# Performance work log

Measured on AMD Instinct MI355X. Metric: run time of the kernel, lower is better.

Reference implementation:

```python
import jax, jax.numpy as jnp
import numpy as np

B = 1024
N_CPGS = 20000
N_FREQS = N_CPGS // 2 + 1  # 10001
HIDDEN = (256, 128, 64)
LN_EPS = 1e-5


def setup_inputs() -> dict:
    key = jax.random.key(0)
    keys = jax.random.split(key, 16)
    inp = {"x": jax.random.normal(keys[0], (B, N_CPGS), dtype=jnp.float32)}
    in_dim = N_FREQS
    for i, h in enumerate(HIDDEN):
        inp[f"W{i}"] = jax.random.normal(keys[1 + i], (h, in_dim), dtype=jnp.float32) * 0.01
        inp[f"alpha{i}"] = jnp.full((h, in_dim), 0.01, dtype=jnp.float32)
        inp[f"b{i}"] = jnp.zeros((h,), dtype=jnp.float32)
        inp[f"eta{i}"] = jnp.asarray(0.1, dtype=jnp.float32)
        inp[f"g{i}"] = jnp.ones((h,), dtype=jnp.float32)   # LayerNorm gamma
        inp[f"be{i}"] = jnp.zeros((h,), dtype=jnp.float32)  # LayerNorm beta
        in_dim = h
    inp["head_w"] = jax.random.normal(keys[10], (1, in_dim), dtype=jnp.float32) * (1.0 / np.sqrt(in_dim))
    inp["head_b"] = jnp.zeros((1,), dtype=jnp.float32)
    return inp


def _hebbian_layer(x, W, alpha, b, eta):
    # y_slow = x W^T + b;  plastic[b,i] = eta * tanh(y_slow)[b,i] * sum_j sigmoid(alpha)[i,j] * x_norm[b,j] * x[b,j]
    y_slow = jnp.einsum('bd,hd->bh', x, W) + b
    x_norm = x / (jnp.linalg.norm(x, axis=-1, keepdims=True) + 1e-8)
    c = x_norm * x  # (B, in) -- collapses the (B,out,in) outer-product trace algebraically
    plastic = eta * jnp.tanh(y_slow) * jnp.einsum('bd,hd->bh', c, jax.nn.sigmoid(alpha))
    return y_slow + plastic


def _layer_norm(h, g, be):
    mu = jnp.mean(h, axis=-1, keepdims=True)
    var = jnp.mean((h - mu) ** 2, axis=-1, keepdims=True)
    return (h - mu) * jax.lax.rsqrt(var + LN_EPS) * g + be


def reference(x, W0, alpha0, b0, eta0, g0, be0,
              W1, alpha1, b1, eta1, g1, be1,
              W2, alpha2, b2, eta2, g2, be2,
              head_w, head_b):
    # FFT spectral front-end
    xc = x - jnp.mean(x, axis=1, keepdims=True)
    h = jnp.log1p(jnp.abs(jnp.fft.rfft(xc, axis=1)))  # (B, N_FREQS)
    params = [(W0, alpha0, b0, eta0, g0, be0),
              (W1, alpha1, b1, eta1, g1, be1),
              (W2, alpha2, b2, eta2, g2, be2)]
    for (W, a, b, eta, g, be) in params:
        h = jax.nn.gelu(_layer_norm(_hebbian_layer(h, W, a, b, eta), g, be), approximate=False)
        # dropout is identity in eval mode
    return (jnp.einsum('bd,od->bo', h, head_w) + head_b)[:, 0]  # (B,)
```

## Files before the change

kernel.cpp:

```cpp
#include <hip/hip_runtime.h>
#include <hip/hip_bf16.h>
#include <math.h>

typedef short bf16x8 __attribute__((ext_vector_type(8)));
typedef float f32x4 __attribute__((ext_vector_type(4)));

static __device__ __forceinline__ unsigned short f2bf(float f) {
    unsigned int u = __float_as_uint(f);
    unsigned int r = (u + 0x7fffu + ((u >> 16) & 1u)) >> 16;
    return (unsigned short)r;
}

static __device__ __forceinline__ bf16x8 sq_bf16x8(bf16x8 a) {
    bf16x8 r;
    #pragma unroll
    for (int i = 0; i < 8; ++i) {
        unsigned int u = ((unsigned int)(unsigned short)a[i]) << 16;
        float f = __uint_as_float(u);
        f *= f;
        r[i] = (short)f2bf(f);
    }
    return r;
}

static __device__ __forceinline__ float gelu_f(float x) {
    return 0.5f * x * (1.f + erff(x * 0.70710678118654752f));
}

static __device__ __forceinline__ void gload_lds16(const void* g, void* l) {
    __builtin_amdgcn_global_load_lds(
        (const __attribute__((address_space(1))) unsigned int*)g,
        (__attribute__((address_space(3))) unsigned int*)l, 16, 0, 0);
}

static __device__ __forceinline__ int ldsmap(int i) { return i + (i >> 6); }

static __device__ __forceinline__ int rev4(int k) {
    int d0 = k % 10; k /= 10;
    int d1 = k % 10; k /= 10;
    int d2 = k % 10; int d3 = k / 10;
    return d0 * 1000 + d1 * 100 + d2 * 10 + d3;
}

__global__ __launch_bounds__(256)
void init_tables_kernel(unsigned int* __restrict__ idxTab, float2* __restrict__ twAll)
{
    int i = blockIdx.x * 256 + threadIdx.x;
    if (i < 10001) {
        int k1 = (i == 10000) ? 0 : i;
        int k2 = (k1 == 0) ? 0 : 10000 - k1;
        unsigned a = (unsigned)ldsmap(rev4(k1));
        unsigned b = (unsigned)ldsmap(rev4(k2));
        idxTab[i] = a | (b << 16);
    }
    if (i < 9990) {
        int m;
        if (i < 9000)       { int t = i / 1000 + 1; int j = i - (t - 1) * 1000; m = j * t; }
        else if (i < 9900)  { int e = i - 9000; int t = e / 100 + 1; int j = e - (t - 1) * 100; m = 10 * j * t; }
        else                { int e = i - 9900; int t = e / 10 + 1;  int j = e - (t - 1) * 10;  m = 100 * j * t; }
        double ang = (double)m * -6.2831853071795864769e-4;
        twAll[i] = make_float2((float)cos(ang), (float)sin(ang));
    }
}

static __device__ __forceinline__ void dft5(
    float a0r, float a0i, float a1r, float a1i, float a2r, float a2i,
    float a3r, float a3i, float a4r, float a4i,
    float* Xr, float* Xi)
{
    const float c1 = 0.30901699437494742f, c2 = -0.80901699437494745f;
    const float s1 = 0.95105651629515357f, s2 = 0.58778525229247312f;
    float t1r = a1r + a4r, t1i = a1i + a4i;
    float d1r = a1r - a4r, d1i = a1i - a4i;
    float t2r = a2r + a3r, t2i = a2i + a3i;
    float d2r = a2r - a3r, d2i = a2i - a3i;
    Xr[0] = a0r + t1r + t2r; Xi[0] = a0i + t1i + t2i;
    float m1r = a0r + c1 * t1r + c2 * t2r, m1i = a0i + c1 * t1i + c2 * t2i;
    float m2r = a0r + c2 * t1r + c1 * t2r, m2i = a0i + c2 * t1i + c1 * t2i;
    float n1r = s1 * d1r + s2 * d2r, n1i = s1 * d1i + s2 * d2i;
    float n2r = s2 * d1r - s1 * d2r, n2i = s2 * d1i - s1 * d2i;
    Xr[1] = m1r + n1i; Xi[1] = m1i - n1r;
    Xr[4] = m1r - n1i; Xi[4] = m1i + n1r;
    Xr[2] = m2r + n2i; Xi[2] = m2i - n2r;
    Xr[3] = m2r - n2i; Xi[3] = m2i + n2r;
}

template<int S>
static __device__ __forceinline__ void radix10_core(
    float* __restrict__ reb, float* __restrict__ imb,
    const float* ar, const float* ai, int base, int j,
    const float2* __restrict__ tw)
{
    constexpr int L  = (S == 0) ? 1000 : (S == 1) ? 100 : (S == 2) ? 10 : 1;
    constexpr bool TW = (S != 3);

    const float WR[5] = {1.f, 0.80901699437494745f, 0.30901699437494742f,
                         -0.30901699437494742f, -0.80901699437494745f};
    const float WI[5] = {0.f, -0.58778525229247312f, -0.95105651629515357f,
                         -0.95105651629515357f, -0.58778525229247312f};

    float Er[5], Ei[5], Or[5], Oi[5];
    dft5(ar[0], ai[0], ar[2], ai[2], ar[4], ai[4], ar[6], ai[6], ar[8], ai[8], Er, Ei);
    dft5(ar[1], ai[1], ar[3], ai[3], ar[5], ai[5], ar[7], ai[7], ar[9], ai[9], Or, Oi);
    #pragma unroll
    for (int k = 1; k < 5; ++k) {
        float tr = Or[k] * WR[k] - Oi[k] * WI[k];
        Oi[k] = Or[k] * WI[k] + Oi[k] * WR[k];
        Or[k] = tr;
    }

    if (TW) {
        float twr[10], twi[10];
        #pragma unroll
        for (int t = 1; t < 10; ++t) {
            float2 w_ = tw[(t - 1) * L + j];
            twr[t] = w_.x; twi[t] = w_.y;
        }
        #pragma unroll
        for (int k = 0; k < 5; ++k) {
            float xr0 = Er[k] + Or[k], xi0 = Ei[k] + Oi[k];
            float xr1 = Er[k] - Or[k], xi1 = Ei[k] - Oi[k];
            int i0 = ldsmap(base + k * L);
            int i1 = ldsmap(base + (k + 5) * L);
            if (k == 0) {
                reb[i0] = xr0;
                imb[i0] = xi0;
            } else {
                reb[i0] = xr0 * twr[k] - xi0 * twi[k];
                imb[i0] = xr0 * twi[k] + xi0 * twr[k];
            }
            reb[i1] = xr1 * twr[k + 5] - xi1 * twi[k + 5];
            imb[i1] = xr1 * twi[k + 5] + xi1 * twr[k + 5];
        }
    } else {
        #pragma unroll
        for (int k = 0; k < 5; ++k) {
            int i0 = ldsmap(base + k * L);
            int i1 = ldsmap(base + (k + 5) * L);
            reb[i0] = Er[k] + Or[k]; imb[i0] = Ei[k] + Oi[k];
            reb[i1] = Er[k] - Or[k]; imb[i1] = Ei[k] - Oi[k];
        }
    }
}

template<int S>
static __device__ __forceinline__ void radix10_stage(
    float* __restrict__ reb, float* __restrict__ imb, int tid,
    const float2* __restrict__ tw)
{
    constexpr int L = (S == 1) ? 100 : (S == 2) ? 10 : 1;
    for (int w = tid; w < 1000; w += 512) {
        int g, j;
        if (S == 3) { g = w; j = 0; }
        else        { g = w / L; j = w - g * L; }
        const int base = g * (10 * L) + j;
        float ar[10], ai[10];
        #pragma unroll
        for (int u = 0; u < 10; ++u) {
            int idx = ldsmap(base + u * L);
            ar[u] = reb[idx];
            ai[u] = imb[idx];
        }
        radix10_core<S>(reb, imb, ar, ai, base, j, tw);
    }
}

__global__ __launch_bounds__(512, 4)
void fft_prep_kernel(const float* __restrict__ x,
                     unsigned short* __restrict__ hb,
                     float* __restrict__ hnorm,
                     const float* __restrict__ W0, const float* __restrict__ A0,
                     unsigned short* __restrict__ Wb, unsigned short* __restrict__ Sb,
                     const float* __restrict__ W1, const float* __restrict__ A1,
                     const float* __restrict__ W2, const float* __restrict__ A2,
                     float* __restrict__ W1T, float* __restrict__ S1T,
                     float* __restrict__ W2T, float* __restrict__ S2T,
                     const unsigned int* __restrict__ idxTab,
                     const float2* __restrict__ twAll)
{
    if (blockIdx.x >= 1024) {
        int idx = (blockIdx.x - 1024) * 512 + threadIdx.x;
        if (idx < 1280128) {
            const bool isW = idx < 640064;
            const int f4 = isW ? idx : idx - 640064;
            const float* src = isW ? W0 : A0;
            unsigned short* dst = isW ? Wb : Sb;
            float4 v = ((const float4*)src)[f4];
            float e[4] = {v.x, v.y, v.z, v.w};
            int flat = f4 * 4;
            int row = flat / 10001;
            int col = flat - row * 10001;
            #pragma unroll
            for (int i = 0; i < 4; ++i) {
                if (col == 10001) { row++; col = 0; }
                float val = isW ? e[i] : 1.f / (1.f + expf(-e[i]));
                dst[(size_t)row * 10240 + col] = f2bf(val);
                col++;
            }
        } else if (idx < 1341312) {
            int i = idx - 1280128;
            int row = i / 239;
            int col = 10001 + (i - row * 239);
            Wb[(size_t)row * 10240 + col] = 0;
            Sb[(size_t)row * 10240 + col] = 0;
        } else if (idx < 1423232) {
            int o = idx - 1341312;
            if (o < 32768) {
                int d = o >> 7, h = o & 127;
                W1T[o] = W1[h * 256 + d];
            } else if (o < 65536) {
                int p = o - 32768;
                int d = p >> 7, h = p & 127;
                S1T[p] = 1.f / (1.f + expf(-A1[h * 256 + d]));
            } else if (o < 73728) {
                int p = o - 65536;
                int d = p >> 6, h = p & 63;
                W2T[p] = W2[h * 128 + d];
            } else {
                int p = o - 73728;
                int d = p >> 6, h = p & 63;
                S2T[p] = 1.f / (1.f + expf(-A2[h * 128 + d]));
            }
        }
        return;
    }

    __shared__ float reb[10156];
    __shared__ float imb[10156];
    __shared__ float redbuf[8];

    const int b = blockIdx.x;
    const int tid = threadIdx.x;
    const int lane = tid & 63;
    const int wv = tid >> 6;

    const float2* T0 = twAll;
    const float2* T1 = twAll + 9000;
    const float2* T2 = twAll + 9900;

    const float2* z2 = (const float2*)(x + (size_t)b * 20000);
    for (int w = tid; w < 1000; w += 512) {
        float ar[10], ai[10];
        #pragma unroll
        for (int u = 0; u < 10; ++u) {
            float2 v = z2[w + u * 1000];
            ar[u] = v.x; ai[u] = v.y;
        }
        radix10_core<0>(reb, imb, ar, ai, w, w, T0);
    }
    __syncthreads();
    radix10_stage<1>(reb, imb, tid, T1);
    __syncthreads();
    radix10_stage<2>(reb, imb, tid, T2);
    __syncthreads();
    radix10_stage<3>(reb, imb, tid, (const float2*)nullptr);
    __syncthreads();

    float ct, st;
    __sincosf((float)tid * -3.14159265358979324e-4f, &st, &ct);
    const float RC = 0.987091579f;
    const float RS = -0.160156842f;
    float sumsq = 0.f;
    unsigned short* hrow = hb + (size_t)b * 10240;
    #pragma unroll
    for (int i = 0; i < 20; ++i) {
        int k = tid + i * 512;
        float hval = 0.f;
        if (k > 0 && k <= 10000) {
            unsigned pp = idxTab[k];
            int i1 = (int)(pp & 0xffffu);
            int i2 = (int)(pp >> 16);
            float zr = reb[i1], zi = imb[i1];
            float wr = reb[i2], wi = imb[i2];
            float er = 0.5f * (zr + wr);
            float ei = 0.5f * (zi - wi);
            float odr = 0.5f * (zi + wi);
            float odi = -0.5f * (zr - wr);
            float xre = er + ct * odr - st * odi;
            float xim = ei + ct * odi + st * odr;
            hval = __logf(1.f + sqrtf(xre * xre + xim * xim));
        }
        hrow[k] = f2bf(hval);
        sumsq += hval * hval;
        float nct = ct * RC - st * RS;
        st = ct * RS + st * RC;
        ct = nct;
    }
    #pragma unroll
    for (int o = 32; o; o >>= 1) sumsq += __shfl_xor(sumsq, o);
    __syncthreads();
    if (lane == 0) redbuf[wv] = sumsq;
    __syncthreads();
    if (tid == 0) {
        float tsq = 0.f;
        #pragma unroll
        for (int i = 0; i < 8; ++i) tsq += redbuf[i];
        hnorm[b] = 1.f / (sqrtf(tsq) + 1e-8f);
    }
}

__global__ __launch_bounds__(256, 3)
void gemm0_kernel(const unsigned short* __restrict__ hb,
                  const unsigned short* __restrict__ Wb, const unsigned short* __restrict__ Sb,
                  float* __restrict__ Py, float* __restrict__ Pp)
{
    __shared__ unsigned short Ah[128 * 64];
    __shared__ unsigned short Bw[64 * 64];
    __shared__ unsigned short Bs[64 * 64];

    const int t = threadIdx.x;
    const int lin = blockIdx.x;
    const int xcd = lin & 7;
    const int sub = lin >> 3;
    const int z = xcd * 2 + (sub & 1);
    const int tile = sub >> 1;
    const int b0 = (tile & 7) * 128;
    const int n0 = (tile >> 3) * 64;

    const int lane = t & 63;
    const int wv = t >> 6;
    const int ml = lane & 15;
    const int q4 = lane >> 4;
    const int s0 = q4 ^ (ml & 7);

    const int sub8 = lane >> 3;
    const int sl = lane & 7;
    const int gsw = sl ^ sub8;

    f32x4 accY[2][4], accP[2][4];
    #pragma unroll
    for (int mt = 0; mt < 2; ++mt)
        #pragma unroll
        for (int nt = 0; nt < 4; ++nt) {
            accY[mt][nt] = (f32x4){0.f, 0.f, 0.f, 0.f};
            accP[mt][nt] = (f32x4){0.f, 0.f, 0.f, 0.f};
        }

    const int kbase = z * 640;

    for (int step = 0; step < 10; ++step) {
        const int k0 = kbase + step * 64;
        __syncthreads();
        #pragma unroll
        for (int j = 0; j < 4; ++j) {
            const int c = wv * 4 + j;
            const size_t go = (size_t)(b0 + c * 8 + sub8) * 10240 + k0 + gsw * 8;
            gload_lds16(&hb[go], &Ah[c * 512]);
        }
        #pragma unroll
        for (int j = 0; j < 2; ++j) {
            const int c = wv * 2 + j;
            const size_t go = (size_t)(n0 + c * 8 + sub8) * 10240 + k0 + gsw * 8;
            gload_lds16(&Wb[go], &Bw[c * 512]);
            gload_lds16(&Sb[go], &Bs[c * 512]);
        }
        __syncthreads();

        #pragma unroll
        for (int kk = 0; kk < 2; ++kk) {
            const int slot = (s0 ^ (kk << 2)) << 3;
            bf16x8 ah[2], ac[2], bw[4], bs[4];
            #pragma unroll
            for (int mt = 0; mt < 2; ++mt) {
                int mrow = wv * 32 + mt * 16 + ml;
                ah[mt] = *(const bf16x8*)&Ah[mrow * 64 + slot];
                ac[mt] = sq_bf16x8(ah[mt]);
            }
            #pragma unroll
            for (int nt = 0; nt < 4; ++nt) {
                int nrow = nt * 16 + ml;
                bw[nt] = *(const bf16x8*)&Bw[nrow * 64 + slot];
                bs[nt] = *(const bf16x8*)&Bs[nrow * 64 + slot];
            }
            #pragma unroll
            for (int mt = 0; mt < 2; ++mt)
                #pragma unroll
                for (int nt = 0; nt < 4; ++nt) {
                    accY[mt][nt] = __builtin_amdgcn_mfma_f32_16x16x32_bf16(ah[mt], bw[nt], accY[mt][nt], 0, 0, 0);
                    accP[mt][nt] = __builtin_amdgcn_mfma_f32_16x16x32_bf16(ac[mt], bs[nt], accP[mt][nt], 0, 0, 0);
                }
        }
    }

    const int rq = q4 * 4;
    #pragma unroll
    for (int mt = 0; mt < 2; ++mt)
        #pragma unroll
        for (int nt = 0; nt < 4; ++nt)
            #pragma unroll
            for (int r = 0; r < 4; ++r) {
                int m = b0 + wv * 32 + mt * 16 + rq + r;
                int n = n0 + nt * 16 + ml;
                size_t o = ((size_t)z * 1024 + m) * 256 + n;
                Py[o] = accY[mt][nt][r];
                Pp[o] = accP[mt][nt][r];
            }
}

__global__ __launch_bounds__(256)
void combine_tail_kernel(const float* __restrict__ Py, const float* __restrict__ Pp,
                 const float* __restrict__ hnorm,
                 const float* __restrict__ b0v, const float* __restrict__ eta0p,
                 const float* __restrict__ g0, const float* __restrict__ be0,
                 const float* __restrict__ W1T, const float* __restrict__ S1T,
                 const float* __restrict__ b1, const float* __restrict__ eta1p,
                 const float* __restrict__ g1, const float* __restrict__ be1,
                 const float* __restrict__ W2T, const float* __restrict__ S2T,
                 const float* __restrict__ b2, const float* __restrict__ eta2p,
                 const float* __restrict__ g2, const float* __restrict__ be2,
                 const float* __restrict__ hw, const float* __restrict__ hbod,
                 float* __restrict__ out)
{
    __shared__ float sh[2][256];
    __shared__ float sc[2][256];
    __shared__ float sv[2][128];
    __shared__ float sh2[2][128];
    __shared__ float sc2[2][128];
    __shared__ float sv2[2][64];
    __shared__ float p2a[2][2][64];
    __shared__ float p2b[2][2][64];
    __shared__ float redA[4][2];
    __shared__ float redB[4][2];

    const int t = threadIdx.x;
    const int b0 = blockIdx.x * 2;
    const int lane = t & 63;
    const int wv = t >> 6;

    const float e0 = eta0p[0];
    const float bias0 = b0v[t];
    float ys[2] = {0.f, 0.f}, ps[2] = {0.f, 0.f};
    #pragma unroll 4
    for (int s = 0; s < 16; ++s)
        #pragma unroll
        for (int r = 0; r < 2; ++r) {
            size_t o = ((size_t)s * 1024 + b0 + r) * 256 + t;
            ys[r] += Py[o];
            ps[r] += Pp[o];
        }
    float v[2];
    #pragma unroll
    for (int r = 0; r < 2; ++r) {
        float p = ps[r] * hnorm[b0 + r];
        float y = ys[r] + bias0;
        v[r] = y + e0 * tanhf(y) * p;
    }

    float s1[2], s2[2];
    #pragma unroll
    for (int r = 0; r < 2; ++r) { s1[r] = v[r]; s2[r] = v[r] * v[r]; }
    #pragma unroll
    for (int o = 32; o; o >>= 1)
        #pragma unroll
        for (int r = 0; r < 2; ++r) { s1[r] += __shfl_xor(s1[r], o); s2[r] += __shfl_xor(s2[r], o); }
    if (lane == 0)
        #pragma unroll
        for (int r = 0; r < 2; ++r) { redA[wv][r] = s1[r]; redB[wv][r] = s2[r]; }
    __syncthreads();

    const float gg = g0[t], bb = be0[t];
    float gl[2], s3[2];
    #pragma unroll
    for (int r = 0; r < 2; ++r) {
        float sum = redA[0][r] + redA[1][r] + redA[2][r] + redA[3][r];
        float sumsq = redB[0][r] + redB[1][r] + redB[2][r] + redB[3][r];
        float mu = sum * (1.f / 256.f);
        float var = sumsq * (1.f / 256.f) - mu * mu;
        float u = (v[r] - mu) * rsqrtf(var + 1e-5f) * gg + bb;
        gl[r] = gelu_f(u);
        s3[r] = gl[r] * gl[r];
    }
    #pragma unroll
    for (int o = 32; o; o >>= 1)
        #pragma unroll
        for (int r = 0; r < 2; ++r) s3[r] += __shfl_xor(s3[r], o);
    __syncthreads();
    if (lane == 0)
        #pragma unroll
        for (int r = 0; r < 2; ++r) redA[wv][r] = s3[r];
    __syncthreads();
    #pragma unroll
    for (int r = 0; r < 2; ++r) {
        float gsq = redA[0][r] + redA[1][r] + redA[2][r] + redA[3][r];
        float inv = 1.f / (sqrtf(gsq) + 1e-8f);
        sh[r][t] = gl[r];
        sc[r][t] = gl[r] * gl[r] * inv;
    }
    __syncthreads();

    const int hcol = t & 127;
    const int r1 = t >> 7;
    float ya = 0.f, pa = 0.f;
    #pragma unroll 8
    for (int d = 0; d < 256; ++d) {
        ya += sh[r1][d] * W1T[d * 128 + hcol];
        pa += sc[r1][d] * S1T[d * 128 + hcol];
    }
    {
        const float e1 = eta1p[0];
        float y = ya + b1[hcol];
        sv[r1][hcol] = y + e1 * tanhf(y) * pa;
    }
    __syncthreads();

    if (wv < 2) {
        int r = wv;
        float v0 = sv[r][lane];
        float v1 = sv[r][lane + 64];
        float s = v0 + v1, sq = v0 * v0 + v1 * v1;
        #pragma unroll
        for (int o = 32; o; o >>= 1) { s += __shfl_xor(s, o); sq += __shfl_xor(sq, o); }
        float mu = s * (1.f / 128.f);
        float var = sq * (1.f / 128.f) - mu * mu;
        float rs = rsqrtf(var + 1e-5f);
        float u0 = (v0 - mu) * rs * g1[lane] + be1[lane];
        float u1 = (v1 - mu) * rs * g1[lane + 64] + be1[lane + 64];
        float ge0 = gelu_f(u0);
        float ge1 = gelu_f(u1);
        float gsq = ge0 * ge0 + ge1 * ge1;
        #pragma unroll
        for (int o = 32; o; o >>= 1) gsq += __shfl_xor(gsq, o);
        float inv = 1.f / (sqrtf(gsq) + 1e-8f);
        sh2[r][lane] = ge0; sh2[r][lane + 64] = ge1;
        sc2[r][lane] = ge0 * ge0 * inv; sc2[r][lane + 64] = ge1 * ge1 * inv;
    }
    __syncthreads();

    {
        const int h2c = t & 63;
        const int r = (t >> 6) & 1;
        const int dh = t >> 7;
        float yb = 0.f, pb = 0.f;
        #pragma unroll 8
        for (int dd = 0; dd < 64; ++dd) {
            int d = dh * 64 + dd;
            yb += sh2[r][d] * W2T[d * 64 + h2c];
            pb += sc2[r][d] * S2T[d * 64 + h2c];
        }
        p2a[dh][r][h2c] = yb;
        p2b[dh][r][h2c] = pb;
    }
    __syncthreads();
    if (t < 128) {
        const int h2c = t & 63;
        const int r = t >> 6;
        const float e2 = eta2p[0];
        float yb = p2a[0][r][h2c] + p2a[1][r][h2c];
        float pb = p2b[0][r][h2c] + p2b[1][r][h2c];
        float y = yb + b2[h2c];
        sv2[r][h2c] = y + e2 * tanhf(y) * pb;
    }
    __syncthreads();

    if (wv < 2) {
        int r = wv;
        float v0 = sv2[r][lane];
        float s = v0, sq = v0 * v0;
        #pragma unroll
        for (int o = 32; o; o >>= 1) { s += __shfl_xor(s, o); sq += __shfl_xor(sq, o); }
        float mu = s * (1.f / 64.f);
        float var = sq * (1.f / 64.f) - mu * mu;
        float rs = rsqrtf(var + 1e-5f);
        float u = (v0 - mu) * rs * g2[lane] + be2[lane];
        float g = gelu_f(u);
        float hc = g * hw[lane];
        #pragma unroll
        for (int o = 32; o; o >>= 1) hc += __shfl_xor(hc, o);
        if (lane == 0) out[b0 + r] = hc + hbod[0];
    }
}

extern "C" void kernel_launch(void* const* d_in, const int* in_sizes, int n_in,
                              void* d_out, int out_size, void* d_ws, size_t ws_size,
                              hipStream_t stream)
{
    const float* x    = (const float*)d_in[0];
    const float* W0   = (const float*)d_in[1];
    const float* A0   = (const float*)d_in[2];
    const float* b0   = (const float*)d_in[3];
    const float* eta0 = (const float*)d_in[4];
    const float* g0   = (const float*)d_in[5];
    const float* be0  = (const float*)d_in[6];
    const float* W1   = (const float*)d_in[7];
    const float* A1   = (const float*)d_in[8];
    const float* b1   = (const float*)d_in[9];
    const float* eta1 = (const float*)d_in[10];
    const float* g1   = (const float*)d_in[11];
    const float* be1  = (const float*)d_in[12];
    const float* W2   = (const float*)d_in[13];
    const float* A2   = (const float*)d_in[14];
    const float* b2   = (const float*)d_in[15];
    const float* eta2 = (const float*)d_in[16];
    const float* g2   = (const float*)d_in[17];
    const float* be2  = (const float*)d_in[18];
    const float* hw   = (const float*)d_in[19];
    const float* hbod = (const float*)d_in[20];
    float* out = (float*)d_out;

    char* w = (char*)d_ws;
    unsigned short* hb  = (unsigned short*)(w + 0);
    unsigned short* Wb0 = (unsigned short*)(w + 20971520);
    unsigned short* Sb0 = (unsigned short*)(w + 26214400);
    float* Py   = (float*)(w + 31457280);
    float* Pp   = (float*)(w + 48234496);
    float* W1T  = (float*)(w + 65011712);
    float* S1T  = (float*)(w + 65142784);
    float* W2T  = (float*)(w + 65273856);
    float* S2T  = (float*)(w + 65306624);
    float* hnm  = (float*)(w + 65339392);
    unsigned int* idxT = (unsigned int*)(w + 65343488);
    float2* twT = (float2*)(w + 65384448);

    hipLaunchKernelGGL(init_tables_kernel, dim3(40), dim3(256), 0, stream, idxT, twT);
    hipLaunchKernelGGL(fft_prep_kernel, dim3(3804), dim3(512), 0, stream,
                       x, hb, hnm, W0, A0, Wb0, Sb0, W1, A1, W2, A2, W1T, S1T, W2T, S2T,
                       idxT, twT);
    hipLaunchKernelGGL(gemm0_kernel, dim3(512), dim3(256), 0, stream, hb, Wb0, Sb0, Py, Pp);
    hipLaunchKernelGGL(combine_tail_kernel, dim3(512), dim3(256), 0, stream, Py, Pp, hnm,
                       b0, eta0, g0, be0, W1T, S1T, b1, eta1, g1, be1,
                       W2T, S2T, b2, eta2, g2, be2, hw, hbod, out);
}
```

Before: 252.2 us.

## Halve split-K factor in gemm0 and shrink M tile to 64 rows

The first-layer GEMM now splits K 8 ways instead of 16, and each block uses a 64x64 output tile with one M sub-tile per wave instead of 128x64. The grid stays at 512 blocks, but partial-sum buffers shrink by half, so the combine kernel reads 8 partials instead of 16 and the workspace layout is repacked. The trade-off is less reuse of B tiles per A row, since each block now loads A and B tiles of equal size for half the MFMAs. Each block also runs a longer K loop of 20 steps.

Result: no change. 255.3 us (+1.2%).

```diff
diff --git a/kernel.cpp b/kernel.cpp
--- a/kernel.cpp
+++ b/kernel.cpp
@@ -304,18 +304,16 @@
                   const unsigned short* __restrict__ Wb, const unsigned short* __restrict__ Sb,
                   float* __restrict__ Py, float* __restrict__ Pp)
 {
-    __shared__ unsigned short Ah[128 * 64];
+    __shared__ unsigned short Ah[64 * 64];
     __shared__ unsigned short Bw[64 * 64];
     __shared__ unsigned short Bs[64 * 64];
 
     const int t = threadIdx.x;
     const int lin = blockIdx.x;
-    const int xcd = lin & 7;
-    const int sub = lin >> 3;
-    const int z = xcd * 2 + (sub & 1);
-    const int tile = sub >> 1;
-    const int b0 = (tile & 7) * 128;
-    const int n0 = (tile >> 3) * 64;
+    const int z = lin & 7;
+    const int tile = lin >> 3;
+    const int b0 = (tile & 15) * 64;
+    const int n0 = (tile >> 4) * 64;
 
     const int lane = t & 63;
     const int wv = t >> 6;
@@ -327,45 +325,36 @@
     const int sl = lane & 7;
     const int gsw = sl ^ sub8;
 
-    f32x4 accY[2][4], accP[2][4];
-    #pragma unroll
-    for (int mt = 0; mt < 2; ++mt)
-        #pragma unroll
-        for (int nt = 0; nt < 4; ++nt) {
-            accY[mt][nt] = (f32x4){0.f, 0.f, 0.f, 0.f};
-            accP[mt][nt] = (f32x4){0.f, 0.f, 0.f, 0.f};
-        }
-
-    const int kbase = z * 640;
-
-    for (int step = 0; step < 10; ++step) {
+    f32x4 accY[4], accP[4];
+    #pragma unroll
+    for (int nt = 0; nt < 4; ++nt) {
+        accY[nt] = (f32x4){0.f, 0.f, 0.f, 0.f};
+        accP[nt] = (f32x4){0.f, 0.f, 0.f, 0.f};
+    }
+
+    const int kbase = z * 1280;
+
+    for (int step = 0; step < 20; ++step) {
         const int k0 = kbase + step * 64;
         __syncthreads();
         #pragma unroll
-        for (int j = 0; j < 4; ++j) {
-            const int c = wv * 4 + j;
-            const size_t go = (size_t)(b0 + c * 8 + sub8) * 10240 + k0 + gsw * 8;
-            gload_lds16(&hb[go], &Ah[c * 512]);
-        }
-        #pragma unroll
         for (int j = 0; j < 2; ++j) {
             const int c = wv * 2 + j;
-            const size_t go = (size_t)(n0 + c * 8 + sub8) * 10240 + k0 + gsw * 8;
-            gload_lds16(&Wb[go], &Bw[c * 512]);
-            gload_lds16(&Sb[go], &Bs[c * 512]);
+            const size_t goA = (size_t)(b0 + c * 8 + sub8) * 10240 + k0 + gsw * 8;
+            gload_lds16(&hb[goA], &Ah[c * 512]);
+            const size_t goB = (size_t)(n0 + c * 8 + sub8) * 10240 + k0 + gsw * 8;
+            gload_lds16(&Wb[goB], &Bw[c * 512]);
+            gload_lds16(&Sb[goB], &Bs[c * 512]);
         }
         __syncthreads();
 
         #pragma unroll
         for (int kk = 0; kk < 2; ++kk) {
             const int slot = (s0 ^ (kk << 2)) << 3;
-            bf16x8 ah[2], ac[2], bw[4], bs[4];
-            #pragma unroll
-            for (int mt = 0; mt < 2; ++mt) {
-                int mrow = wv * 32 + mt * 16 + ml;
-                ah[mt] = *(const bf16x8*)&Ah[mrow * 64 + slot];
-                ac[mt] = sq_bf16x8(ah[mt]);
-            }
+            bf16x8 ah, ac, bw[4], bs[4];
+            const int mrow = wv * 16 + ml;
+            ah = *(const bf16x8*)&Ah[mrow * 64 + slot];
+            ac = sq_bf16x8(ah);
             #pragma unroll
             for (int nt = 0; nt < 4; ++nt) {
                 int nrow = nt * 16 + ml;
@@ -373,28 +362,24 @@
                 bs[nt] = *(const bf16x8*)&Bs[nrow * 64 + slot];
             }
             #pragma unroll
-            for (int mt = 0; mt < 2; ++mt)
-                #pragma unroll
-                for (int nt = 0; nt < 4; ++nt) {
-                    accY[mt][nt] = __builtin_amdgcn_mfma_f32_16x16x32_bf16(ah[mt], bw[nt], accY[mt][nt], 0, 0, 0);
-                    accP[mt][nt] = __builtin_amdgcn_mfma_f32_16x16x32_bf16(ac[mt], bs[nt], accP[mt][nt], 0, 0, 0);
-                }
+            for (int nt = 0; nt < 4; ++nt) {
+                accY[nt] = __builtin_amdgcn_mfma_f32_16x16x32_bf16(ah, bw[nt], accY[nt], 0, 0, 0);
+                accP[nt] = __builtin_amdgcn_mfma_f32_16x16x32_bf16(ac, bs[nt], accP[nt], 0, 0, 0);
+            }
         }
     }
 
     const int rq = q4 * 4;
     #pragma unroll
-    for (int mt = 0; mt < 2; ++mt)
-        #pragma unroll
-        for (int nt = 0; nt < 4; ++nt)
-            #pragma unroll
-            for (int r = 0; r < 4; ++r) {
-                int m = b0 + wv * 32 + mt * 16 + rq + r;
-                int n = n0 + nt * 16 + ml;
-                size_t o = ((size_t)z * 1024 + m) * 256 + n;
-                Py[o] = accY[mt][nt][r];
-                Pp[o] = accP[mt][nt][r];
-            }
+    for (int nt = 0; nt < 4; ++nt)
+        #pragma unroll
+        for (int r = 0; r < 4; ++r) {
+            int m = b0 + wv * 16 + rq + r;
+            int n = n0 + nt * 16 + ml;
+            size_t o = ((size_t)z * 1024 + m) * 256 + n;
+            Py[o] = accY[nt][r];
+            Pp[o] = accP[nt][r];
+        }
 }
 
 __global__ __launch_bounds__(256)
@@ -431,7 +416,7 @@
     const float bias0 = b0v[t];
     float ys[2] = {0.f, 0.f}, ps[2] = {0.f, 0.f};
     #pragma unroll 4
-    for (int s = 0; s < 16; ++s)
+    for (int s = 0; s < 8; ++s)
         #pragma unroll
         for (int r = 0; r < 2; ++r) {
             size_t o = ((size_t)s * 1024 + b0 + r) * 256 + t;
@@ -602,14 +587,14 @@
     unsigned short* Wb0 = (unsigned short*)(w + 20971520);
     unsigned short* Sb0 = (unsigned short*)(w + 26214400);
     float* Py   = (float*)(w + 31457280);
-    float* Pp   = (float*)(w + 48234496);
-    float* W1T  = (float*)(w + 65011712);
-    float* S1T  = (float*)(w + 65142784);
-    float* W2T  = (float*)(w + 65273856);
-    float* S2T  = (float*)(w + 65306624);
-    float* hnm  = (float*)(w + 65339392);
-    unsigned int* idxT = (unsigned int*)(w + 65343488);
-    float2* twT = (float2*)(w + 65384448);
+    float* Pp   = (float*)(w + 39845888);
+    float* W1T  = (float*)(w + 48234496);
+    float* S1T  = (float*)(w + 48365568);
+    float* W2T  = (float*)(w + 48496640);
+    float* S2T  = (float*)(w + 48529408);
+    float* hnm  = (float*)(w + 48562176);
+    unsigned int* idxT = (unsigned int*)(w + 48566272);
+    float2* twT = (float2*)(w + 48607232);
 
     hipLaunchKernelGGL(init_tables_kernel, dim3(40), dim3(256), 0, stream, idxT, twT);
     hipLaunchKernelGGL(fft_prep_kernel, dim3(3804), dim3(512), 0, stream,
```
